# Optimization experiments

Measured on AMD Instinct MI355X. Metric: run time of the kernel, lower is better.

Reference implementation:

```python
import jax, jax.numpy as jnp
import numpy as np

LMAX = 8                         # lmax-1 used by s2/so3 irreps
DIMS = [2 * l + 1 for l in range(LMAX + 1)]
S2_OFF = np.cumsum([0] + DIMS).tolist()            # offsets into 81-dim s2 irreps
SO3_OFF = np.cumsum([0] + [d * d for d in DIMS]).tolist()  # offsets into 969-dim so3 irreps
S2_DIM = S2_OFF[-1]              # 81
SO3_DIM = SO3_OFF[-1]            # 969
F_IN = 81                        # multiplicity into S2Conv
F_SO3 = 300
C = 768                          # encoder feature channels
KS = 7                           # encoder feature map / kernel size
B = 8
G_S2 = 48                        # s2 healpix grid rec_level=1
G_ACT = 4096                     # SO3Activation grid points (stand-in for res=20 grid)
G_SO3 = 36864                    # so3 healpix grid rec_level=3


def setup_inputs() -> dict:
    key = jax.random.key(0)
    ks = jax.random.split(key, 7)
    return {
        "x": jax.random.normal(ks[0], (B, C, KS, KS), jnp.float32),
        "F": jax.random.normal(ks[1], (F_IN, S2_DIM * C, KS, KS), jnp.float32) * 0.02,
        "w_s2": jax.random.normal(ks[2], (F_IN, F_SO3, G_S2), jnp.float32) * 0.1,
        "Y": jax.random.normal(ks[3], (G_S2, S2_DIM), jnp.float32),
        "w_so3": jax.random.normal(ks[4], (F_SO3, 1, G_SO3), jnp.float32) * 0.1,
        "D": jax.random.normal(ks[5], (G_SO3, SO3_DIM), jnp.float32),
        "D_act": jax.random.normal(ks[6], (G_ACT, SO3_DIM), jnp.float32),
    }


def _forward(x, F, w_s2, Y, w_so3, D, D_act):
    b = x.shape[0]
    # ---- Induction layer: split expanded R2Conv filter into 768-channel chunks,
    # stack, contract with feature map. g_split: (n=81, c_out=81, C, 7, 7)
    g = jnp.swapaxes(F.reshape(F_IN, S2_DIM, C, KS, KS), 0, 1)
    y = jnp.einsum('ijkhw,akhw->aji', g, x)          # (B, 81, 81): (batch, f_in, s2 irreps)

    # ---- S2Conv: expand kernel into irrep space, per-l block linear (s2 -> so3 irreps)
    psi = jnp.einsum('ni,xyn->xyi', Y, w_s2) / np.sqrt(G_S2)  # (81, 300, 81)
    outs = []
    for l, d in enumerate(DIMS):
        o = S2_OFF[l]
        xl = y[:, :, o:o + d]                        # (B, f_in, 2l+1)
        wl = psi[:, :, o:o + d]                      # (f_in, f_out, mul_out=2l+1)
        ol = jnp.einsum('bfm,fgu->bgum', xl, wl) / np.sqrt(F_IN)
        outs.append(ol.reshape(b, F_SO3, d * d))
    z = jnp.concatenate(outs, axis=-1)               # (B, 300, 969)

    # ---- SO3Activation: to grid, relu, back to irreps
    s = jnp.einsum('bfi,gi->bfg', z, D_act)
    z = jnp.einsum('bfg,gi->bfi', jax.nn.relu(s), D_act) / G_ACT

    # ---- SO3Conv: expand kernel via Wigner-D buffer, per-l block linear (so3 -> so3)
    psi2 = jnp.einsum('ni,xyn->xyi', D, w_so3) / np.sqrt(G_SO3)  # (300, 1, 969)
    outs = []
    for l, d in enumerate(DIMS):
        o = SO3_OFF[l]
        xl = z[:, :, o:o + d * d].reshape(b, F_SO3, d, d)   # (B, f, u, m)
        wl = psi2[:, :, o:o + d * d].reshape(F_SO3, 1, d, d)  # (f, g, v, u)
        ol = jnp.einsum('bfum,fgvu->bgvm', xl, wl) / np.sqrt(F_SO3 * d)
        outs.append(ol.reshape(b, 1, d * d))
    return jnp.concatenate(outs, axis=-1)            # (B, 1, 969)


def reference(x, F, w_s2, Y, w_so3, D, D_act):
    return _forward(x, F, w_s2, Y, w_so3, D, D_act)
```

## Files before the change

kernel.cpp:

```cpp
#include <hip/hip_runtime.h>
#include <hip/hip_bf16.h>
#include <math.h>

#define THREADS 256

constexpr int B_    = 8;
constexpr int C_    = 768;
constexpr int KS_   = 7;
constexpr int F_IN  = 81;
constexpr int F_SO3 = 300;
constexpr int S2_DIM  = 81;
constexpr int SO3_DIM = 969;
constexpr int G_S2  = 48;
constexpr int G_ACT = 4096;
constexpr int G_SO3 = 36864;
constexpr int CKK   = C_ * KS_ * KS_;
constexpr int CKK4  = CKK / 4;
constexpr int NPAIR = F_IN * S2_DIM;

constexpr int D2_SPLIT = 8;
constexpr int E1_SPLIT = 32;
constexpr int F_SPLIT  = 5;

__constant__ int d_S2_OFF[10]  = {0, 1, 4, 9, 16, 25, 36, 49, 64, 81};
__constant__ int d_SO3_OFF[10] = {0, 1, 10, 35, 84, 165, 286, 455, 680, 969};

struct CEnt { unsigned char u, m, so, l; };
struct CLut { CEnt v[992]; };
constexpr CLut make_clut() {
  CLut t{};
  int S2O[10]  = {0, 1, 4, 9, 16, 25, 36, 49, 64, 81};
  int SO3O[10] = {0, 1, 10, 35, 84, 165, 286, 455, 680, 969};
  for (int i = 0; i < 969; ++i) {
    int l = 0;
    while (i >= SO3O[l + 1]) ++l;
    int d = 2 * l + 1, r = i - SO3O[l];
    t.v[i].u  = (unsigned char)(r / d);
    t.v[i].m  = (unsigned char)(r % d);
    t.v[i].so = (unsigned char)S2O[l];
    t.v[i].l  = (unsigned char)l;
  }
  return t;
}
__constant__ CLut g_clut = make_clut();

using short8 = __attribute__((ext_vector_type(8))) short;
using f32x4  = __attribute__((ext_vector_type(4))) float;
using f4v    = __attribute__((ext_vector_type(4))) float;

#define GL16(gp, lp)                                                        \
  __builtin_amdgcn_global_load_lds(                                         \
      (const __attribute__((address_space(1))) void*)(gp),                  \
      (__attribute__((address_space(3))) void*)(lp), 16, 0, 0)

constexpr size_t AL(size_t x) { return (x + 1023) & ~(size_t)1023; }
constexpr size_t O_Y     = 0;
constexpr size_t O_PSI   = O_Y     + AL((size_t)8 * NPAIR * 4);
constexpr size_t O_ZBF   = O_PSI   + AL((size_t)F_IN * F_SO3 * 81 * 4);
constexpr size_t O_DACT  = O_ZBF   + AL((size_t)2432 * 1024 * 2);
constexpr size_t O_DACTT = O_DACT  + AL((size_t)4096 * 1024 * 2);
constexpr size_t O_WSO3  = O_DACTT + AL((size_t)1024 * 4096 * 2);
constexpr size_t O_DT    = O_WSO3  + AL((size_t)384 * 36864 * 2);
constexpr size_t O_SBF   = O_DT    + AL((size_t)1024 * 36864 * 2);
constexpr size_t O_D2P   = O_SBF   + AL((size_t)2432 * 4096 * 2);
constexpr size_t O_E1P   = O_D2P   + AL((size_t)D2_SPLIT * 2432 * 1024 * 4);
constexpr size_t O_PSI2  = O_E1P   + AL((size_t)E1_SPLIT * 384 * 1024 * 4);
constexpr size_t O_SFP   = O_PSI2  + AL((size_t)F_SO3 * SO3_DIM * 4);
constexpr size_t FAST_NEED = O_SFP + AL((size_t)F_SPLIT * 8 * SO3_DIM * 4);

constexpr size_t WS_Y    = 0;
constexpr size_t WS_PSI  = 52488;
constexpr size_t WS_Z    = 2020788;
constexpr size_t WS_S    = 4346388;
constexpr size_t WS_Z2   = 14176788;
constexpr size_t WS_P2P  = 16502388;
constexpr size_t WS_PSI2 = 18827988;

__device__ __forceinline__ void stage_a_body(
    const float* __restrict__ Fm, const float* __restrict__ x, float* __restrict__ y,
    char* smemc, int blk) {
  const int p0  = blk * 3;
  const int tid = threadIdx.x;
  const f4v* __restrict__ F4 = (const f4v*)Fm;
  const f4v* __restrict__ x4 = (const f4v*)x;

  float acc[3][8];
#pragma unroll
  for (int p = 0; p < 3; ++p)
#pragma unroll
    for (int b = 0; b < 8; ++b) acc[p][b] = 0.f;

  for (int i = tid; i < CKK4; i += THREADS) {
    f4v xv[8];
#pragma unroll
    for (int b = 0; b < 8; ++b) xv[b] = x4[b * CKK4 + i];
#pragma unroll
    for (int p = 0; p < 3; ++p) {
      f4v fv = __builtin_nontemporal_load(&F4[(size_t)(p0 + p) * CKK4 + i]);
#pragma unroll
      for (int b = 0; b < 8; ++b)
        acc[p][b] += fv[0] * xv[b][0] + fv[1] * xv[b][1] + fv[2] * xv[b][2] + fv[3] * xv[b][3];
    }
  }

  float (*red)[24] = (float(*)[24])smemc;
  const int lane = tid & 63, wid = tid >> 6;
#pragma unroll
  for (int p = 0; p < 3; ++p) {
#pragma unroll
    for (int b = 0; b < 8; ++b) {
      float v = acc[p][b];
      v += __shfl_down(v, 32);
      v += __shfl_down(v, 16);
      v += __shfl_down(v, 8);
      v += __shfl_down(v, 4);
      v += __shfl_down(v, 2);
      v += __shfl_down(v, 1);
      if (lane == 0) red[wid][p * 8 + b] = v;
    }
  }
  __syncthreads();
  if (tid < 24) {
    float v = red[0][tid] + red[1][tid] + red[2][tid] + red[3][tid];
    int p = tid / 8, b = tid % 8;
    y[(size_t)b * NPAIR + p0 + p] = v;
  }
}

__device__ __forceinline__ void cvt4_body(const float* __restrict__ src,
                                          __hip_bfloat16* __restrict__ dst,
                                          int R, int Cs, int Cp, int blk) {
  size_t e0 = ((size_t)blk * THREADS + threadIdx.x) * 4;
  int r = (int)(e0 / (unsigned)Cp), c = (int)(e0 % (unsigned)Cp);
  __hip_bfloat16 o[4];
#pragma unroll
  for (int j = 0; j < 4; ++j) {
    float v = (r < R && c + j < Cs) ? src[(size_t)r * Cs + c + j] : 0.f;
    o[j] = __float2bfloat16(v);
  }
  *(ushort4*)(&dst[e0]) = *(const ushort4*)o;
}

__device__ __forceinline__ void tr_body(const float* __restrict__ src,
                                        __hip_bfloat16* __restrict__ dst,
                                        int R, int Cs, size_t dstStride, int bx, int by,
                                        char* smemc) {
  float (*tile)[33] = (float(*)[33])smemc;
  const int c0 = bx * 32, r0 = by * 32;
  const int tx = threadIdx.x & 31, ty = threadIdx.x >> 5;
#pragma unroll
  for (int i = 0; i < 32; i += 8) {
    int r = r0 + ty + i, c = c0 + tx;
    tile[ty + i][tx] = (c < Cs) ? src[(size_t)r * Cs + c] : 0.f;
  }
  __syncthreads();
  const int rp = threadIdx.x & 15;
  const int cl = threadIdx.x >> 4;
#pragma unroll
  for (int j = 0; j < 2; ++j) {
    int cc = cl + 16 * j;
    int c  = c0 + cc;
    if (c < Cs) {
      __hip_bfloat16 o[2];
      o[0] = __float2bfloat16(tile[2 * rp][cc]);
      o[1] = __float2bfloat16(tile[2 * rp + 1][cc]);
      *(ushort2*)(&dst[(size_t)c * dstStride + r0 + 2 * rp]) = *(const ushort2*)o;
    }
  }
}

__device__ __forceinline__ void psi_body(const float* __restrict__ w_s2,
                                         const float* __restrict__ Y,
                                         float* __restrict__ psi_t, int blk) {
  int idx = blk * THREADS + threadIdx.x;
  if (idx >= F_IN * F_SO3 * S2_DIM) return;
  int s  = idx % S2_DIM;
  int t1 = idx / S2_DIM;
  int f  = t1 % F_IN;
  int g  = t1 / F_IN;
  const float* w = w_s2 + ((size_t)f * F_SO3 + g) * G_S2;
  float acc = 0.f;
#pragma unroll 8
  for (int n = 0; n < G_S2; ++n) acc += w[n] * Y[n * S2_DIM + s];
  psi_t[idx] = acc * 0.14433756729740643f;
}

constexpr int UB1 = 4096;
constexpr int UB2 = 3968;
constexpr int UB3 = 13824;
constexpr int UB4 = 35712;
constexpr int UB5 = 7689;
constexpr int UB_TOT = UB1 + UB2 + UB3 + UB4 + UB5;

__global__ __launch_bounds__(THREADS) void k_uber(
    const float* __restrict__ D_act, __hip_bfloat16* __restrict__ Dact_bf,
    __hip_bfloat16* __restrict__ DactT_bf,
    const float* __restrict__ w_so3, __hip_bfloat16* __restrict__ wso3_bf,
    const float* __restrict__ D, __hip_bfloat16* __restrict__ DT_bf,
    const float* __restrict__ w_s2, const float* __restrict__ Y, float* __restrict__ psi_t) {
  __shared__ __align__(16) char smem[4352];
  int b = blockIdx.x;
  if (b < UB1) { cvt4_body(D_act, Dact_bf, G_ACT, SO3_DIM, 1024, b); return; }
  b -= UB1;
  if (b < UB2) { tr_body(D_act, DactT_bf, G_ACT, SO3_DIM, 4096, b % 31, b / 31, smem); return; }
  b -= UB2;
  if (b < UB3) { cvt4_body(w_so3, wso3_bf, F_SO3, G_SO3, G_SO3, b); return; }
  b -= UB3;
  if (b < UB4) { tr_body(D, DT_bf, G_SO3, SO3_DIM, 36864, b % 31, b / 31, smem); return; }
  b -= UB4;
  psi_body(w_s2, Y, psi_t, b);
}

__global__ __launch_bounds__(THREADS) void k_stage_c_bf(
    const float* __restrict__ y, const float* __restrict__ psi_t,
    __hip_bfloat16* __restrict__ z) {
  const int b = blockIdx.x / F_SO3;
  const int g = blockIdx.x % F_SO3;
  __shared__ float ybl[NPAIR];
  __shared__ float psl[NPAIR];
  const int tid = threadIdx.x;
  const float* pg = psi_t + (size_t)g * NPAIR;
  for (int t = tid; t < NPAIR; t += THREADS) {
    ybl[t] = y[(size_t)b * NPAIR + t];
    psl[t] = pg[t];
  }
  __syncthreads();
  for (int i = tid; i < 1024; i += THREADS) {
    float acc = 0.f;
    if (i < SO3_DIM) {
      CEnt e = g_clut.v[i];
      int im = e.so + e.m, iu = e.so + e.u;
#pragma unroll 9
      for (int f = 0; f < F_IN; ++f)
        acc += ybl[f * S2_DIM + im] * psl[f * S2_DIM + iu];
      acc *= (1.0f / 9.0f);
    }
    z[((size_t)b * F_SO3 + g) * 1024 + i] = __float2bfloat16(acc);
  }
}

struct GemmDesc {
  const __hip_bfloat16* A;
  const __hip_bfloat16* B;
  void* C;
  int K, kSpan, Ncols;
  float scale;
  size_t splitStride;
  int gx, gy, gz, epi;
};

__device__ __forceinline__ void mfma_nt_body(const GemmDesc g, unsigned lin, char* smem) {
  char* As = smem;
  char* Bs = smem + 16384;

  unsigned nwg = (unsigned)(g.gx * g.gy * g.gz);
  if ((nwg & 7u) == 0u) {
    unsigned q = nwg >> 3;
    lin = (lin & 7u) * q + (lin >> 3);
  }
  const int bxi = (int)(lin % (unsigned)g.gx);
  const unsigned t1 = lin / (unsigned)g.gx;
  const int byi = (int)(t1 % (unsigned)g.gy);
  const int bzi = (int)(t1 / (unsigned)g.gy);

  const int t    = threadIdx.x;
  const int lane = t & 63;
  const int wave = t >> 6;
  const int wr   = wave >> 1, wc = wave & 1;
  const int bm = byi * 128, bn = bxi * 128;
  const int kBegin = bzi * g.kSpan;
  const int kEnd   = kBegin + g.kSpan;

  const char* pA[4];
  const char* pB[4];
  int ldsOff[4];
#pragma unroll
  for (int i = 0; i < 4; ++i) {
    int L   = i * 4096 + t * 16;
    int row = L >> 7;
    int kb  = (L & 127) ^ ((row & 7) << 4);
    pA[i] = (const char*)g.A + ((size_t)(bm + row) * g.K) * 2 + kb;
    pB[i] = (const char*)g.B + ((size_t)(bn + row) * g.K) * 2 + kb;
    ldsOff[i] = L;
  }

  f32x4 acc[4][4] = {};

  for (int k0 = kBegin; k0 < kEnd; k0 += 64) {
    size_t koff = (size_t)k0 * 2;
#pragma unroll
    for (int i = 0; i < 4; ++i) {
      GL16(pA[i] + koff, As + ldsOff[i]);
      GL16(pB[i] + koff, Bs + ldsOff[i]);
    }
    __syncthreads();
#pragma unroll
    for (int kk = 0; kk < 2; ++kk) {
      const int klin = kk * 64 + ((lane >> 4) << 4);
      short8 af[4], bfr[4];
#pragma unroll
      for (int m = 0; m < 4; ++m) {
        int ra = (wr << 6) + (m << 4) + (lane & 15);
        af[m] = *(const short8*)(As + ra * 128 + (klin ^ ((ra & 7) << 4)));
        int rb = (wc << 6) + (m << 4) + (lane & 15);
        bfr[m] = *(const short8*)(Bs + rb * 128 + (klin ^ ((rb & 7) << 4)));
      }
#pragma unroll
      for (int m = 0; m < 4; ++m)
#pragma unroll
        for (int n = 0; n < 4; ++n)
          acc[m][n] = __builtin_amdgcn_mfma_f32_16x16x32_bf16(af[m], bfr[n], acc[m][n], 0, 0, 0);
    }
    __syncthreads();
  }

  const int rbase = bm + (wr << 6) + ((lane >> 4) << 2);
  const int cbase = bn + (wc << 6) + (lane & 15);
  if (g.epi == 0) {
    float* C = (float*)g.C + (size_t)bzi * g.splitStride;
#pragma unroll
    for (int m = 0; m < 4; ++m)
#pragma unroll
      for (int n = 0; n < 4; ++n)
#pragma unroll
        for (int r = 0; r < 4; ++r)
          C[(size_t)(rbase + m * 16 + r) * g.Ncols + (cbase + n * 16)] = acc[m][n][r] * g.scale;
  } else {
    __hip_bfloat16* C = (__hip_bfloat16*)g.C;
#pragma unroll
    for (int m = 0; m < 4; ++m)
#pragma unroll
      for (int n = 0; n < 4; ++n)
#pragma unroll
        for (int r = 0; r < 4; ++r)
          C[(size_t)(rbase + m * 16 + r) * g.Ncols + (cbase + n * 16)] =
              __float2bfloat16(fmaxf(acc[m][n][r], 0.f));
  }
}

__global__ __launch_bounds__(THREADS) void k_mfma_dual(GemmDesc g0, GemmDesc g1, int n0) {
  __shared__ __align__(16) char smem[32768];
  if ((int)blockIdx.x < n0) mfma_nt_body(g0, blockIdx.x, smem);
  else                      mfma_nt_body(g1, blockIdx.x - n0, smem);
}

__global__ __launch_bounds__(THREADS) void k_mfma_reduce(
    GemmDesc g, int n0,
    const float* __restrict__ parts, float* __restrict__ dst, int R, int C,
    size_t rowStride, size_t splitStride, size_t dstStride, int nSplit, float scale) {
  __shared__ __align__(16) char smem[32768];
  if ((int)blockIdx.x < n0) { mfma_nt_body(g, blockIdx.x, smem); return; }
  int idx = (int)(blockIdx.x - n0) * THREADS + threadIdx.x;
  if (idx >= R * C) return;
  int r = idx / C, c = idx % C;
  float a = 0.f;
  for (int s = 0; s < nSplit; ++s) a += parts[(size_t)s * splitStride + (size_t)r * rowStride + c];
  dst[(size_t)r * dstStride + c] = a * scale;
}

__global__ __launch_bounds__(THREADS) void k_stage_f_part(
    const float* __restrict__ d2p, const float* __restrict__ psi2, float* __restrict__ partial) {
  const int b  = blockIdx.x / 9;
  const int l  = blockIdx.x % 9;
  const int sp = blockIdx.y;
  const int d = 2 * l + 1, d2 = d * d;
  const int off = d_SO3_OFF[l];
  constexpr size_t SS = (size_t)2432 * 1024;
  __shared__ float zb[10][289];
  __shared__ float pb[10][289];
  const int tid = threadIdx.x;
  float acc[2] = {0.f, 0.f};
  const int fBeg = sp * (F_SO3 / F_SPLIT), fEnd = fBeg + F_SO3 / F_SPLIT;
  for (int fc = fBeg; fc < fEnd; fc += 10) {
    for (int t = tid; t < 10 * d2; t += THREADS) {
      int fl = t / d2, q = t - fl * d2;
      int f  = fc + fl;
      size_t zi = ((size_t)b * F_SO3 + f) * 1024 + off + q;
      float zv = 0.f;
#pragma unroll
      for (int s = 0; s < D2_SPLIT; ++s) zv += d2p[zi + (size_t)s * SS];
      zb[fl][q] = zv * (1.0f / G_ACT);
      pb[fl][q] = psi2[(size_t)f * SO3_DIM + off + q];
    }
    __syncthreads();
#pragma unroll 2
    for (int io = 0; io < 2; ++io) {
      int i = tid + io * THREADS;
      if (i < d2) {
        int v = i / d, m = i - v * d;
        float a = acc[io];
#pragma unroll
        for (int fl = 0; fl < 10; ++fl) {
          float s_ = 0.f;
          for (int u = 0; u < d; ++u)
            s_ += zb[fl][u * d + m] * pb[fl][v * d + u];
          a += s_;
        }
        acc[io] = a;
      }
    }
    __syncthreads();
  }
  for (int io = 0; io < 2; ++io) {
    int i = tid + io * THREADS;
    if (i < d2) partial[((size_t)sp * 8 + b) * SO3_DIM + off + i] = acc[io];
  }
}

__global__ __launch_bounds__(THREADS) void k_stage_f_red(
    const float* __restrict__ partial, float* __restrict__ out) {
  int idx = blockIdx.x * THREADS + threadIdx.x;
  if (idx >= 8 * SO3_DIM) return;
  int b = idx / SO3_DIM, i = idx % SO3_DIM;
  int l = g_clut.v[i].l;
  float a = 0.f;
#pragma unroll
  for (int sp = 0; sp < F_SPLIT; ++sp)
    a += partial[((size_t)sp * 8 + b) * SO3_DIM + i];
  out[(size_t)b * SO3_DIM + i] = a * rsqrtf(300.0f * (float)(2 * l + 1));
}

__global__ __launch_bounds__(THREADS) void k_stage_a3(
    const float* __restrict__ Fm, const float* __restrict__ x, float* __restrict__ y) {
  __shared__ __align__(16) char smem[512];
  stage_a_body(Fm, x, y, smem, blockIdx.x);
}

__global__ __launch_bounds__(THREADS) void k_psi(
    const float* __restrict__ w_s2, const float* __restrict__ Y, float* __restrict__ psi_t) {
  psi_body(w_s2, Y, psi_t, blockIdx.x);
}

__global__ __launch_bounds__(THREADS) void k_stage_c(
    const float* __restrict__ y, const float* __restrict__ psi_t, float* __restrict__ z) {
  const int b = blockIdx.x / F_SO3;
  const int g = blockIdx.x % F_SO3;
  __shared__ float ybl[NPAIR];
  __shared__ float psl[NPAIR];
  const int tid = threadIdx.x;
  const float* pg = psi_t + (size_t)g * NPAIR;
  for (int t = tid; t < NPAIR; t += THREADS) {
    ybl[t] = y[(size_t)b * NPAIR + t];
    psl[t] = pg[t];
  }
  __syncthreads();
  for (int i = tid; i < SO3_DIM; i += THREADS) {
    CEnt e = g_clut.v[i];
    int im = e.so + e.m, iu = e.so + e.u;
    float acc = 0.f;
#pragma unroll 9
    for (int f = 0; f < F_IN; ++f)
      acc += ybl[f * S2_DIM + im] * psl[f * S2_DIM + iu];
    z[((size_t)b * F_SO3 + g) * SO3_DIM + i] = acc * (1.0f / 9.0f);
  }
}

__global__ __launch_bounds__(THREADS) void k_gemm_nt_relu(
    const float* __restrict__ A, const float* __restrict__ Bm, float* __restrict__ Cm,
    int M, int N, int K) {
  __shared__ float As[16][68];
  __shared__ float Bs[16][68];
  const int bm = blockIdx.y * 64, bn = blockIdx.x * 64;
  const int t  = threadIdx.x;
  const int lk = t & 15, lm = t >> 4;
  const int tn = t & 15, tm = t >> 4;
  float acc[4][4] = {};
  for (int k0 = 0; k0 < K; k0 += 16) {
    int gk = k0 + lk;
#pragma unroll
    for (int j = 0; j < 4; ++j) {
      int m  = lm + 16 * j;
      int gm = bm + m;
      As[lk][m] = (gm < M && gk < K) ? A[(size_t)gm * K + gk] : 0.f;
      int gn = bn + m;
      Bs[lk][m] = (gn < N && gk < K) ? Bm[(size_t)gn * K + gk] : 0.f;
    }
    __syncthreads();
#pragma unroll
    for (int k = 0; k < 16; ++k) {
      float4 av = *(const float4*)&As[k][tm * 4];
      float4 bv = *(const float4*)&Bs[k][tn * 4];
      float a[4] = {av.x, av.y, av.z, av.w};
      float bb[4] = {bv.x, bv.y, bv.z, bv.w};
#pragma unroll
      for (int i2 = 0; i2 < 4; ++i2)
#pragma unroll
        for (int j2 = 0; j2 < 4; ++j2)
          acc[i2][j2] += a[i2] * bb[j2];
    }
    __syncthreads();
  }
#pragma unroll
  for (int i2 = 0; i2 < 4; ++i2) {
    int gm = bm + tm * 4 + i2;
    if (gm >= M) continue;
#pragma unroll
    for (int j2 = 0; j2 < 4; ++j2) {
      int gn = bn + tn * 4 + j2;
      if (gn < N) Cm[(size_t)gm * N + gn] = fmaxf(acc[i2][j2], 0.f);
    }
  }
}

__global__ __launch_bounds__(THREADS) void k_gemm_nn(
    const float* __restrict__ A, const float* __restrict__ Bm, float* __restrict__ Cm,
    int M, int N, int K, int kSpan, float scale, size_t cStride) {
  __shared__ float As[16][68];
  __shared__ float Bs[16][68];
  const int bm = blockIdx.y * 64, bn = blockIdx.x * 64;
  const int t   = threadIdx.x;
  const int lk  = t & 15, lm = t >> 4;
  const int ln  = t & 63, lkq = t >> 6;
  const int tn  = t & 15, tm = t >> 4;
  const int kBegin = blockIdx.z * kSpan;
  const int kEnd   = kBegin + kSpan;
  float* C = Cm + (size_t)blockIdx.z * cStride;
  float acc[4][4] = {};
  for (int k0 = kBegin; k0 < kEnd; k0 += 16) {
    {
      int gk = k0 + lk;
#pragma unroll
      for (int j = 0; j < 4; ++j) {
        int m = lm + 16 * j, gm = bm + m;
        As[lk][m] = (gm < M) ? A[(size_t)gm * K + gk] : 0.f;
      }
    }
    {
      int gn = bn + ln;
#pragma unroll
      for (int j = 0; j < 4; ++j) {
        int k = lkq + 4 * j;
        Bs[k][ln] = (gn < N) ? Bm[(size_t)(k0 + k) * N + gn] : 0.f;
      }
    }
    __syncthreads();
#pragma unroll
    for (int k = 0; k < 16; ++k) {
      float4 av = *(const float4*)&As[k][tm * 4];
      float4 bv = *(const float4*)&Bs[k][tn * 4];
      float a[4] = {av.x, av.y, av.z, av.w};
      float bb[4] = {bv.x, bv.y, bv.z, bv.w};
#pragma unroll
      for (int i2 = 0; i2 < 4; ++i2)
#pragma unroll
        for (int j2 = 0; j2 < 4; ++j2)
          acc[i2][j2] += a[i2] * bb[j2];
    }
    __syncthreads();
  }
#pragma unroll
  for (int i2 = 0; i2 < 4; ++i2) {
    int gm = bm + tm * 4 + i2;
    if (gm >= M) continue;
#pragma unroll
    for (int j2 = 0; j2 < 4; ++j2) {
      int gn = bn + tn * 4 + j2;
      if (gn < N) C[(size_t)gm * N + gn] = acc[i2][j2] * scale;
    }
  }
}

__global__ __launch_bounds__(THREADS) void k_reduce_psi2(
    const float* __restrict__ parts, float* __restrict__ psi2) {
  int idx = blockIdx.x * THREADS + threadIdx.x;
  if (idx >= F_SO3 * SO3_DIM) return;
  float acc = 0.f;
#pragma unroll
  for (int s = 0; s < 8; ++s) acc += parts[(size_t)s * (F_SO3 * SO3_DIM) + idx];
  psi2[idx] = acc * (1.0f / 192.0f);
}

__global__ __launch_bounds__(THREADS) void k_stage_f(
    const float* __restrict__ z2, const float* __restrict__ psi2, float* __restrict__ out,
    int zStride) {
  const int b = blockIdx.x / 9;
  const int l = blockIdx.x % 9;
  const int d = 2 * l + 1, d2 = d * d;
  const int off = d_SO3_OFF[l];
  __shared__ float zb[10][289];
  __shared__ float pb[10][289];
  const int tid = threadIdx.x;
  float acc[2] = {0.f, 0.f};
  const float scale = rsqrtf(300.0f * (float)d);
  for (int fc = 0; fc < F_SO3; fc += 10) {
    for (int t = tid; t < 10 * d2; t += THREADS) {
      int fl = t / d2, q = t - fl * d2;
      int f  = fc + fl;
      zb[fl][q] = z2[((size_t)b * F_SO3 + f) * zStride + off + q];
      pb[fl][q] = psi2[(size_t)f * SO3_DIM + off + q];
    }
    __syncthreads();
#pragma unroll 2
    for (int io = 0; io < 2; ++io) {
      int i = tid + io * THREADS;
      if (i < d2) {
        int v = i / d, m = i - v * d;
        float a = acc[io];
#pragma unroll
        for (int fl = 0; fl < 10; ++fl) {
          float s_ = 0.f;
          for (int u = 0; u < d; ++u)
            s_ += zb[fl][u * d + m] * pb[fl][v * d + u];
          a += s_;
        }
        acc[io] = a;
      }
    }
    __syncthreads();
  }
  for (int io = 0; io < 2; ++io) {
    int i = tid + io * THREADS;
    if (i < d2) out[(size_t)b * SO3_DIM + off + i] = acc[io] * scale;
  }
}

extern "C" void kernel_launch(void* const* d_in, const int* in_sizes, int n_in,
                              void* d_out, int out_size, void* d_ws, size_t ws_size,
                              hipStream_t stream) {
  const float* x     = (const float*)d_in[0];
  const float* Fm    = (const float*)d_in[1];
  const float* w_s2  = (const float*)d_in[2];
  const float* Y     = (const float*)d_in[3];
  const float* w_so3 = (const float*)d_in[4];
  const float* D     = (const float*)d_in[5];
  const float* D_act = (const float*)d_in[6];
  float* out = (float*)d_out;

  if (ws_size >= FAST_NEED) {
    char* p = (char*)d_ws;
    float*          y       = (float*)(p + O_Y);
    float*          psi     = (float*)(p + O_PSI);
    __hip_bfloat16* z_bf    = (__hip_bfloat16*)(p + O_ZBF);
    __hip_bfloat16* Dact_bf = (__hip_bfloat16*)(p + O_DACT);
    __hip_bfloat16* DactT_bf= (__hip_bfloat16*)(p + O_DACTT);
    __hip_bfloat16* wso3_bf = (__hip_bfloat16*)(p + O_WSO3);
    __hip_bfloat16* DT_bf   = (__hip_bfloat16*)(p + O_DT);
    __hip_bfloat16* s_bf    = (__hip_bfloat16*)(p + O_SBF);
    float*          d2p     = (float*)(p + O_D2P);
    float*          e1p     = (float*)(p + O_E1P);
    float*          psi2    = (float*)(p + O_PSI2);
    float*          sfp     = (float*)(p + O_SFP);

    k_stage_a3<<<NPAIR / 3, THREADS, 0, stream>>>(Fm, x, y);
    k_uber<<<UB_TOT, THREADS, 0, stream>>>(
        D_act, Dact_bf, DactT_bf, w_so3, wso3_bf, D, DT_bf, w_s2, Y, psi);
    k_stage_c_bf<<<B_ * F_SO3, THREADS, 0, stream>>>(y, psi, z_bf);

    GemmDesc e1{wso3_bf, DT_bf, e1p, G_SO3, G_SO3 / E1_SPLIT, 1024, 1.f,
                (size_t)384 * 1024, 8, 3, E1_SPLIT, 0};
    GemmDesc d1{z_bf, Dact_bf, s_bf, 1024, 1024, 4096, 1.f, 0, 32, 19, 1, 1};
    int nE1 = 8 * 3 * E1_SPLIT;
    int nD1 = 32 * 19;
    k_mfma_dual<<<nE1 + nD1, THREADS, 0, stream>>>(e1, d1, nE1);

    GemmDesc d2{s_bf, DactT_bf, d2p, 4096, 4096 / D2_SPLIT, 1024, 1.f,
                (size_t)2432 * 1024, 8, 19, D2_SPLIT, 0};
    int nD2 = 8 * 19 * D2_SPLIT;
    int nE1r = (F_SO3 * SO3_DIM + THREADS - 1) / THREADS;
    k_mfma_reduce<<<nD2 + nE1r, THREADS, 0, stream>>>(
        d2, nD2, e1p, psi2, F_SO3, SO3_DIM, 1024, (size_t)384 * 1024, SO3_DIM,
        E1_SPLIT, 1.0f / 192.0f);

    k_stage_f_part<<<dim3(B_ * 9, F_SPLIT), THREADS, 0, stream>>>(d2p, psi2, sfp);
    k_stage_f_red<<<(8 * SO3_DIM + THREADS - 1) / THREADS, THREADS, 0, stream>>>(sfp, out);
  } else {
    float* ws  = (float*)d_ws;
    float* y    = ws + WS_Y;
    float* psi  = ws + WS_PSI;
    float* z    = ws + WS_Z;
    float* s    = ws + WS_S;
    float* z2   = ws + WS_Z2;
    float* p2p  = ws + WS_P2P;
    float* psi2 = ws + WS_PSI2;

    k_stage_a3<<<NPAIR / 3, THREADS, 0, stream>>>(Fm, x, y);
    k_psi<<<(F_IN * F_SO3 * S2_DIM + THREADS - 1) / THREADS, THREADS, 0, stream>>>(w_s2, Y, psi);
    k_stage_c<<<B_ * F_SO3, THREADS, 0, stream>>>(y, psi, z);
    k_gemm_nt_relu<<<dim3(G_ACT / 64, (B_ * F_SO3 + 63) / 64), THREADS, 0, stream>>>(
        z, D_act, s, B_ * F_SO3, G_ACT, SO3_DIM);
    k_gemm_nn<<<dim3((SO3_DIM + 63) / 64, (B_ * F_SO3 + 63) / 64, 1), THREADS, 0, stream>>>(
        s, D_act, z2, B_ * F_SO3, SO3_DIM, G_ACT, G_ACT, 1.0f / G_ACT, 0);
    k_gemm_nn<<<dim3((SO3_DIM + 63) / 64, (F_SO3 + 63) / 64, 8), THREADS, 0, stream>>>(
        w_so3, D, p2p, F_SO3, SO3_DIM, G_SO3, G_SO3 / 8, 1.0f, (size_t)F_SO3 * SO3_DIM);
    k_reduce_psi2<<<(F_SO3 * SO3_DIM + THREADS - 1) / THREADS, THREADS, 0, stream>>>(p2p, psi2);
    k_stage_f<<<B_ * 9, THREADS, 0, stream>>>(z2, psi2, out, SO3_DIM);
  }
}
```

Before: 612.2 us.

## Rewrite bf16 MFMA GEMM as 128x256 tile with triple-buffered async LDS pipeline

```diff
diff --git a/kernel.cpp b/kernel.cpp
--- a/kernel.cpp
+++ b/kernel.cpp
@@ -18,8 +18,8 @@
 constexpr int CKK4  = CKK / 4;
 constexpr int NPAIR = F_IN * S2_DIM;
 
-constexpr int D2_SPLIT = 8;
-constexpr int E1_SPLIT = 32;
+constexpr int D2_SPLIT = 4;
+constexpr int E1_SPLIT = 24;
 constexpr int F_SPLIT  = 5;
 
 __constant__ int d_S2_OFF[10]  = {0, 1, 4, 9, 16, 25, 36, 49, 64, 81};
@@ -53,6 +53,14 @@
       (const __attribute__((address_space(1))) void*)(gp),                  \
       (__attribute__((address_space(3))) void*)(lp), 16, 0, 0)
 
+#define WAIT_VMCNT6() asm volatile("s_waitcnt vmcnt(6)" ::: "memory")
+#define BARRIER()                                   \
+  do {                                              \
+    __builtin_amdgcn_sched_barrier(0);              \
+    __builtin_amdgcn_s_barrier();                   \
+    __builtin_amdgcn_sched_barrier(0);              \
+  } while (0)
+
 constexpr size_t AL(size_t x) { return (x + 1023) & ~(size_t)1023; }
 constexpr size_t O_Y     = 0;
 constexpr size_t O_PSI   = O_Y     + AL((size_t)8 * NPAIR * 4);
@@ -125,6 +133,12 @@
     int p = tid / 8, b = tid % 8;
     y[(size_t)b * NPAIR + p0 + p] = v;
   }
+}
+
+__global__ __launch_bounds__(THREADS) void k_stage_a3(
+    const float* __restrict__ Fm, const float* __restrict__ x, float* __restrict__ y) {
+  __shared__ __align__(16) char smem[512];
+  stage_a_body(Fm, x, y, smem, blockIdx.x);
 }
 
 __device__ __forceinline__ void cvt4_body(const float* __restrict__ src,
@@ -239,7 +253,7 @@
   }
 }
 
-struct GemmDesc {
+struct G256 {
   const __hip_bfloat16* A;
   const __hip_bfloat16* B;
   void* C;
@@ -249,10 +263,7 @@
   int gx, gy, gz, epi;
 };
 
-__device__ __forceinline__ void mfma_nt_body(const GemmDesc g, unsigned lin, char* smem) {
-  char* As = smem;
-  char* Bs = smem + 16384;
-
+__device__ __forceinline__ void mfma256_body(const G256& g, unsigned lin, char* smem) {
   unsigned nwg = (unsigned)(g.gx * g.gy * g.gz);
   if ((nwg & 7u) == 0u) {
     unsigned q = nwg >> 3;
@@ -265,53 +276,100 @@
 
   const int t    = threadIdx.x;
   const int lane = t & 63;
-  const int wave = t >> 6;
-  const int wr   = wave >> 1, wc = wave & 1;
-  const int bm = byi * 128, bn = bxi * 128;
+  const int wid  = t >> 6;
+  const int wr   = wid >> 2, wc = wid & 3;
+  const int bm = byi * 128, bn = bxi * 256;
   const int kBegin = bzi * g.kSpan;
-  const int kEnd   = kBegin + g.kSpan;
-
-  const char* pA[4];
-  const char* pB[4];
-  int ldsOff[4];
-#pragma unroll
-  for (int i = 0; i < 4; ++i) {
-    int L   = i * 4096 + t * 16;
+  const int NG = g.kSpan >> 6;
+
+  int aL[2], bL[4];
+  const char* aSrc[2];
+  const char* bSrc[4];
+#pragma unroll
+  for (int i = 0; i < 2; ++i) {
+    int L = (i * 512 + t) * 16;
     int row = L >> 7;
     int kb  = (L & 127) ^ ((row & 7) << 4);
-    pA[i] = (const char*)g.A + ((size_t)(bm + row) * g.K) * 2 + kb;
-    pB[i] = (const char*)g.B + ((size_t)(bn + row) * g.K) * 2 + kb;
-    ldsOff[i] = L;
-  }
+    aL[i] = L;
+    aSrc[i] = (const char*)g.A + ((size_t)(bm + row) * g.K) * 2 + kb;
+  }
+#pragma unroll
+  for (int i = 0; i < 4; ++i) {
+    int L = (i * 512 + t) * 16;
+    int row = L >> 7;
+    int kb  = (L & 127) ^ ((row & 7) << 4);
+    bL[i] = L;
+    bSrc[i] = (const char*)g.B + ((size_t)(bn + row) * g.K) * 2 + kb;
+  }
+
+  auto STAGE = [&](int buf, int kt) {
+    size_t ko = (size_t)(kBegin + (kt << 6)) * 2;
+    char* Ab = smem + buf * 49152;
+    char* Bb = Ab + 16384;
+#pragma unroll
+    for (int i = 0; i < 2; ++i) GL16(aSrc[i] + ko, Ab + aL[i]);
+#pragma unroll
+    for (int i = 0; i < 4; ++i) GL16(bSrc[i] + ko, Bb + bL[i]);
+  };
 
   f32x4 acc[4][4] = {};
 
-  for (int k0 = kBegin; k0 < kEnd; k0 += 64) {
-    size_t koff = (size_t)k0 * 2;
-#pragma unroll
-    for (int i = 0; i < 4; ++i) {
-      GL16(pA[i] + koff, As + ldsOff[i]);
-      GL16(pB[i] + koff, Bs + ldsOff[i]);
-    }
-    __syncthreads();
-#pragma unroll
-    for (int kk = 0; kk < 2; ++kk) {
-      const int klin = kk * 64 + ((lane >> 4) << 4);
-      short8 af[4], bfr[4];
-#pragma unroll
-      for (int m = 0; m < 4; ++m) {
-        int ra = (wr << 6) + (m << 4) + (lane & 15);
-        af[m] = *(const short8*)(As + ra * 128 + (klin ^ ((ra & 7) << 4)));
-        int rb = (wc << 6) + (m << 4) + (lane & 15);
-        bfr[m] = *(const short8*)(Bs + rb * 128 + (klin ^ ((rb & 7) << 4)));
-      }
-#pragma unroll
-      for (int m = 0; m < 4; ++m)
-#pragma unroll
-        for (int n = 0; n < 4; ++n)
-          acc[m][n] = __builtin_amdgcn_mfma_f32_16x16x32_bf16(af[m], bfr[n], acc[m][n], 0, 0, 0);
-    }
-    __syncthreads();
+  STAGE(0, 0);
+  STAGE(1, 1);
+  WAIT_VMCNT6();
+  BARRIER();
+
+  int bi = 0;
+  for (int gg = 0; gg < NG; ++gg) {
+    char* Ab = smem + bi * 49152;
+    char* Bb = Ab + 16384;
+    short8 af[4], bf[4];
+
+#pragma unroll
+    for (int m = 0; m < 4; ++m) {
+      int ra = (wr << 6) + (m << 4) + (lane & 15);
+      af[m] = *(const short8*)(Ab + ra * 128 + ((((lane >> 4) << 4)) ^ ((ra & 7) << 4)));
+    }
+#pragma unroll
+    for (int n = 0; n < 4; ++n) {
+      int rb = (wc << 6) + (n << 4) + (lane & 15);
+      bf[n] = *(const short8*)(Bb + rb * 128 + ((((lane >> 4) << 4)) ^ ((rb & 7) << 4)));
+    }
+    BARRIER();
+    __builtin_amdgcn_s_setprio(1);
+#pragma unroll
+    for (int m = 0; m < 4; ++m)
+#pragma unroll
+      for (int n = 0; n < 4; ++n)
+        acc[m][n] = __builtin_amdgcn_mfma_f32_16x16x32_bf16(af[m], bf[n], acc[m][n], 0, 0, 0);
+    __builtin_amdgcn_s_setprio(0);
+
+#pragma unroll
+    for (int m = 0; m < 4; ++m) {
+      int ra = (wr << 6) + (m << 4) + (lane & 15);
+      af[m] = *(const short8*)(Ab + ra * 128 + ((64 + ((lane >> 4) << 4)) ^ ((ra & 7) << 4)));
+    }
+#pragma unroll
+    for (int n = 0; n < 4; ++n) {
+      int rb = (wc << 6) + (n << 4) + (lane & 15);
+      bf[n] = *(const short8*)(Bb + rb * 128 + ((64 + ((lane >> 4) << 4)) ^ ((rb & 7) << 4)));
+    }
+    {
+      int b2 = bi + 2; if (b2 >= 3) b2 -= 3;
+      int kt2 = (gg + 2 < NG) ? gg + 2 : 0;
+      STAGE(b2, kt2);
+    }
+    WAIT_VMCNT6();
+    BARRIER();
+    __builtin_amdgcn_s_setprio(1);
+#pragma unroll
+    for (int m = 0; m < 4; ++m)
+#pragma unroll
+      for (int n = 0; n < 4; ++n)
+        acc[m][n] = __builtin_amdgcn_mfma_f32_16x16x32_bf16(af[m], bf[n], acc[m][n], 0, 0, 0);
+    __builtin_amdgcn_s_setprio(0);
+
+    if (++bi == 3) bi = 0;
   }
 
   const int rbase = bm + (wr << 6) + ((lane >> 4) << 2);
@@ -338,24 +396,24 @@
   }
 }
 
-__global__ __launch_bounds__(THREADS) void k_mfma_dual(GemmDesc g0, GemmDesc g1, int n0) {
-  __shared__ __align__(16) char smem[32768];
-  if ((int)blockIdx.x < n0) mfma_nt_body(g0, blockIdx.x, smem);
-  else                      mfma_nt_body(g1, blockIdx.x - n0, smem);
-}
-
-__global__ __launch_bounds__(THREADS) void k_mfma_reduce(
-    GemmDesc g, int n0,
-    const float* __restrict__ parts, float* __restrict__ dst, int R, int C,
-    size_t rowStride, size_t splitStride, size_t dstStride, int nSplit, float scale) {
-  __shared__ __align__(16) char smem[32768];
-  if ((int)blockIdx.x < n0) { mfma_nt_body(g, blockIdx.x, smem); return; }
-  int idx = (int)(blockIdx.x - n0) * THREADS + threadIdx.x;
-  if (idx >= R * C) return;
-  int r = idx / C, c = idx % C;
+__global__ __launch_bounds__(512) void k_g256_dual(G256 g0, G256 g1, int n0) {
+  __shared__ __align__(16) char smem[147456];
+  if ((int)blockIdx.x < n0) mfma256_body(g0, blockIdx.x, smem);
+  else                      mfma256_body(g1, blockIdx.x - n0, smem);
+}
+
+__global__ __launch_bounds__(512) void k_g256_d2_e1r(
+    G256 g, int n0,
+    const float* __restrict__ parts, float* __restrict__ psi2) {
+  __shared__ __align__(16) char smem[147456];
+  if ((int)blockIdx.x < n0) { mfma256_body(g, blockIdx.x, smem); return; }
+  int idx = (int)(blockIdx.x - n0) * 512 + threadIdx.x;
+  if (idx >= F_SO3 * SO3_DIM) return;
+  int r = idx / SO3_DIM, c = idx % SO3_DIM;
   float a = 0.f;
-  for (int s = 0; s < nSplit; ++s) a += parts[(size_t)s * splitStride + (size_t)r * rowStride + c];
-  dst[(size_t)r * dstStride + c] = a * scale;
+#pragma unroll 8
+  for (int s = 0; s < E1_SPLIT; ++s) a += parts[(size_t)s * (384 * 1024) + (size_t)r * 1024 + c];
+  psi2[(size_t)r * SO3_DIM + c] = a * (1.0f / 192.0f);
 }
 
 __global__ __launch_bounds__(THREADS) void k_stage_f_part(
@@ -420,12 +478,6 @@
   out[(size_t)b * SO3_DIM + i] = a * rsqrtf(300.0f * (float)(2 * l + 1));
 }
 
-__global__ __launch_bounds__(THREADS) void k_stage_a3(
-    const float* __restrict__ Fm, const float* __restrict__ x, float* __restrict__ y) {
-  __shared__ __align__(16) char smem[512];
-  stage_a_body(Fm, x, y, smem, blockIdx.x);
-}
-
 __global__ __launch_bounds__(THREADS) void k_psi(
     const float* __restrict__ w_s2, const float* __restrict__ Y, float* __restrict__ psi_t) {
   psi_body(w_s2, Y, psi_t, blockIdx.x);
@@ -646,20 +698,18 @@
         D_act, Dact_bf, DactT_bf, w_so3, wso3_bf, D, DT_bf, w_s2, Y, psi);
     k_stage_c_bf<<<B_ * F_SO3, THREADS, 0, stream>>>(y, psi, z_bf);
 
-    GemmDesc e1{wso3_bf, DT_bf, e1p, G_SO3, G_SO3 / E1_SPLIT, 1024, 1.f,
-                (size_t)384 * 1024, 8, 3, E1_SPLIT, 0};
-    GemmDesc d1{z_bf, Dact_bf, s_bf, 1024, 1024, 4096, 1.f, 0, 32, 19, 1, 1};
-    int nE1 = 8 * 3 * E1_SPLIT;
-    int nD1 = 32 * 19;
-    k_mfma_dual<<<nE1 + nD1, THREADS, 0, stream>>>(e1, d1, nE1);
-
-    GemmDesc d2{s_bf, DactT_bf, d2p, 4096, 4096 / D2_SPLIT, 1024, 1.f,
-                (size_t)2432 * 1024, 8, 19, D2_SPLIT, 0};
-    int nD2 = 8 * 19 * D2_SPLIT;
-    int nE1r = (F_SO3 * SO3_DIM + THREADS - 1) / THREADS;
-    k_mfma_reduce<<<nD2 + nE1r, THREADS, 0, stream>>>(
-        d2, nD2, e1p, psi2, F_SO3, SO3_DIM, 1024, (size_t)384 * 1024, SO3_DIM,
-        E1_SPLIT, 1.0f / 192.0f);
+    G256 e1{wso3_bf, DT_bf, e1p, G_SO3, G_SO3 / E1_SPLIT, 1024, 1.f,
+            (size_t)384 * 1024, 4, 3, E1_SPLIT, 0};
+    G256 d1{z_bf, Dact_bf, s_bf, 1024, 1024, 4096, 1.f, 0, 16, 19, 1, 1};
+    int nE1 = 4 * 3 * E1_SPLIT;
+    int nD1 = 16 * 19;
+    k_g256_dual<<<nE1 + nD1, 512, 0, stream>>>(e1, d1, nE1);
+
+    G256 d2{s_bf, DactT_bf, d2p, 4096, 4096 / D2_SPLIT, 1024, 1.f,
+            (size_t)2432 * 1024, 4, 19, D2_SPLIT, 0};
+    int nD2  = 4 * 19 * D2_SPLIT;
+    int nE1r = (F_SO3 * SO3_DIM + 511) / 512;
+    k_g256_d2_e1r<<<nD2 + nE1r, 512, 0, stream>>>(d2, nD2, e1p, psi2);
 
     k_stage_f_part<<<dim3(B_ * 9, F_SPLIT), THREADS, 0, stream>>>(d2p, psi2, sfp);
     k_stage_f_red<<<(8 * SO3_DIM + THREADS - 1) / THREADS, THREADS, 0, stream>>>(sfp, out);
```

New measurement: 558.7 us, median of 2. 8.7% less time.
